# Kernel tuning notes

Measured on AMD Instinct MI355X. Metric: run time of the kernel, lower is better.

Reference implementation:

```python
import jax, jax.numpy as jnp
import numpy as np

N_NODES = 40000
N_EDGES = 640000
C = 128        # in_channels == hidden_channels
H = 8          # heads
D = C // H     # head dim = 16
L = 2          # num HGTConv layers
OUT = 64       # final fc out_channels


def _segment_softmax(logits, seg, num_segments):
    # logits: [E, H], seg: [E] destination ids
    m = jax.ops.segment_max(logits, seg, num_segments=num_segments)
    m = jnp.where(jnp.isfinite(m), m, 0.0)  # empty segments -> 0
    e = jnp.exp(logits - m[seg])
    s = jax.ops.segment_sum(e, seg, num_segments=num_segments)
    return e / (s[seg] + 1e-16)


def setup_inputs() -> dict:
    key = jax.random.key(0)
    ks = jax.random.split(key, 20)
    p = lambda k, shape, s=0.05: (jax.random.normal(k, shape, jnp.float32) * s)
    x = jax.random.normal(ks[0], (N_NODES, C), jnp.float32)
    edge_index = jax.random.randint(ks[1], (2, N_EDGES), 0, N_NODES, jnp.int64)
    return {
        "x": x,
        "edge_index": edge_index,
        # per-layer stacked params (all layers have C->C dims)
        "Wk": p(ks[2], (L, C, C)), "bk": jnp.zeros((L, C), jnp.float32),
        "Wq": p(ks[3], (L, C, C)), "bq": jnp.zeros((L, C), jnp.float32),
        "Wv": p(ks[4], (L, C, C)), "bv": jnp.zeros((L, C), jnp.float32),
        "a_rel": p(ks[5], (L, H, D, D), 0.1),  # relation key transform
        "m_rel": p(ks[6], (L, H, D, D), 0.1),  # relation message transform
        "p_rel": jnp.ones((L, H), jnp.float32),  # relation prior per head
        "skip": jnp.ones((L,), jnp.float32),      # skip gate logits
        "aW": p(ks[7], (L, C, C)), "ab": jnp.zeros((L, C), jnp.float32),
        "fcW": p(ks[8], (C, OUT)), "fcb": jnp.zeros((OUT,), jnp.float32),
    }


def reference(x, edge_index, Wk, bk, Wq, bq, Wv, bv, a_rel, m_rel, p_rel, skip,
              aW, ab, fcW, fcb):
    src, dst = edge_index[0], edge_index[1]
    n = x.shape[0]
    n_layers, heads, d = a_rel.shape[0], a_rel.shape[1], a_rel.shape[2]
    inv_sqrt_d = 1.0 / np.sqrt(d).astype(np.float32)

    h = x
    for l in range(n_layers):
        k = (h @ Wk[l] + bk[l]).reshape(n, heads, d)
        q = (h @ Wq[l] + bq[l]).reshape(n, heads, d)
        v = (h @ Wv[l] + bv[l]).reshape(n, heads, d)
        # relation-specific transforms applied at node level (single edge type)
        k2 = jnp.einsum('nhd,hde->nhe', k, a_rel[l])
        v2 = jnp.einsum('nhd,hde->nhe', v, m_rel[l])
        # per-edge attention logits [E, H]
        logits = jnp.sum(q[dst] * k2[src], axis=-1) * p_rel[l] * inv_sqrt_d
        alpha = _segment_softmax(logits, dst, n)                 # [E, H]
        msg = v2[src] * alpha[:, :, None]                        # [E, H, D]
        agg = jax.ops.segment_sum(msg, dst, num_segments=n)      # [N, H, D]
        agg = agg.reshape(n, heads * d)
        a = jax.nn.gelu(agg) @ aW[l] + ab[l]
        beta = jax.nn.sigmoid(skip[l])
        h = beta * a + (1.0 - beta) * h     # HGT skip (dims match)
        h = jax.nn.relu(h)                  # model-level relu
    return h @ fcW + fcb
```

## Files before the change

### kernel.cpp

```cpp
#include <hip/hip_runtime.h>
#include <hip/hip_bf16.h>
#include <math.h>

#define NN 40000
#define NE 640000

typedef __attribute__((ext_vector_type(8))) short short8;
typedef __attribute__((ext_vector_type(8))) unsigned short u16x8;
typedef __attribute__((ext_vector_type(4))) float f32x4;
typedef _Float16 h16x2 __attribute__((ext_vector_type(2)));

#define WBLOCKS 547
#define GBLOCKS 625
#define NCO 157
#define P1B 160
#define EPB 4000
#define NH (NCO*P1B)
#define NHB 99

#if __has_builtin(__builtin_amdgcn_fdot2)
#define HAS_FDOT2 1
#else
#define HAS_FDOT2 0
#endif

__device__ __forceinline__ float gelu_tanh(float x) {
    float x3 = x * x * x;
    float u = 0.7978845608028654f * (x + 0.044715f * x3);
    return 0.5f * x * (1.0f + tanhf(u));
}

__device__ __forceinline__ unsigned short f2bf(float v) {
    __hip_bfloat16 h = __float2bfloat16(v);
    return *reinterpret_cast<unsigned short*>(&h);
}

__device__ __forceinline__ unsigned short f2h(float v) {
    union { _Float16 h; unsigned short u; } c;
    c.h = (_Float16)v;
    return c.u;
}

__device__ __forceinline__ float bf2f(unsigned short u) {
    union { unsigned int i; float f; } c;
    c.i = ((unsigned int)u) << 16;
    return c.f;
}

__device__ __forceinline__ void unpack8(u16x8 u, float* f) {
    union { u16x8 v; unsigned int d[4]; } c; c.v = u;
    #pragma unroll
    for (int i = 0; i < 4; ++i) {
        union { unsigned int i_; float f_; } lo, hi;
        lo.i_ = c.d[i] << 16;
        hi.i_ = c.d[i] & 0xffff0000u;
        f[2 * i] = lo.f_;
        f[2 * i + 1] = hi.f_;
    }
}

union kv8 { u16x8 u; h16x2 p[4]; _Float16 h[8]; };
union frag8 { short8 s; unsigned short u[8]; u16x8 v; };

__global__ __launch_bounds__(256) void prep_kernel(
    const float* __restrict__ Wq, const float* __restrict__ bq,
    const float* __restrict__ Wk, const float* __restrict__ bk,
    const float* __restrict__ a_rel,
    const float* __restrict__ Wv, const float* __restrict__ bv,
    const float* __restrict__ m_rel,
    const float* __restrict__ p_rel,
    const float* __restrict__ aW, const float* __restrict__ fcW,
    unsigned short* __restrict__ BfT, float* __restrict__ biasf,
    unsigned short* __restrict__ aWT, unsigned short* __restrict__ fcWT,
    const int* __restrict__ eidx, int* __restrict__ Hmat)
{
    if (blockIdx.x >= WBLOCKS) {
        __shared__ int chist[NCO];
        int b = blockIdx.x - WBLOCKS;
        int t = threadIdx.x;
        if (t < NCO) chist[t] = 0;
        __syncthreads();
        int base = b * EPB;
        for (int e = base + t; e < base + EPB; e += 256)
            atomicAdd(&chist[eidx[NE + e] >> 8], 1);
        __syncthreads();
        if (t < NCO) Hmat[t * P1B + b] = chist[t];
        return;
    }
    int idx = blockIdx.x * 256 + threadIdx.x;
    if (idx < 2 * 129 * 384) {
        int l = idx / (129 * 384);
        int j = idx - l * (129 * 384);
        int r = j / 384;
        int col = j - r * 384;
        const float* Wq_l = Wq + l * 16384;
        const float* Wk_l = Wk + l * 16384;
        const float* Wv_l = Wv + l * 16384;
        const float* ar_l = a_rel + l * 2048;
        const float* mr_l = m_rel + l * 2048;
        float val;
        if (col < 128) {
            val = (r < 128) ? Wq_l[r * 128 + col] : bq[l * 128 + col];
        } else if (col < 256) {
            int cc = col - 128; int h = cc >> 4; int eo = cc & 15;
            float scale = p_rel[l * 8 + h] * 0.25f * 1.4426950408889634f;
            float s = 0.f;
            #pragma unroll
            for (int d = 0; d < 16; ++d) {
                float w = (r < 128) ? Wk_l[r * 128 + h * 16 + d] : bk[l * 128 + h * 16 + d];
                s += w * ar_l[h * 256 + d * 16 + eo];
            }
            val = s * scale;
        } else {
            int cc = col - 256; int h = cc >> 4; int eo = cc & 15;
            float s = 0.f;
            #pragma unroll
            for (int d = 0; d < 16; ++d) {
                float w = (r < 128) ? Wv_l[r * 128 + h * 16 + d] : bv[l * 128 + h * 16 + d];
                s += w * mr_l[h * 256 + d * 16 + eo];
            }
            val = s;
        }
        if (r < 128) BfT[(size_t)l * 49152 + (size_t)col * 128 + r] = f2bf(val);
        else         biasf[l * 384 + col] = val;
    } else if (idx < 2 * 129 * 384 + 2 * 16384) {
        int i = idx - 2 * 129 * 384;
        int l = i >> 14; int j = i & 16383;
        int r = j >> 7, c = j & 127;
        aWT[(size_t)l * 16384 + (size_t)c * 128 + r] = f2bf(aW[(size_t)l * 16384 + r * 128 + c]);
    } else {
        int i = idx - (2 * 129 * 384 + 2 * 16384);
        int c = i >> 7, r = i & 127;
        fcWT[(size_t)c * 128 + r] = f2bf(fcW[(size_t)r * 64 + c]);
    }
}

__global__ __launch_bounds__(256) void scan_blocks_kernel(
    const int* __restrict__ in, int* __restrict__ out, int* __restrict__ bsum)
{
    __shared__ int s[256];
    int t = threadIdx.x;
    int i = blockIdx.x * 256 + t;
    int v = (i < NH) ? in[i] : 0;
    s[t] = v;
    __syncthreads();
    #pragma unroll
    for (int off = 1; off < 256; off <<= 1) {
        int u = (t >= off) ? s[t - off] : 0;
        __syncthreads();
        s[t] += u;
        __syncthreads();
    }
    if (i < NH) out[i] = s[t] - v;
    if (t == 255) bsum[blockIdx.x] = s[255];
}

__global__ __launch_bounds__(256) void scan_top_kernel(
    const int* __restrict__ bsum, int* __restrict__ boffs)
{
    __shared__ int s[256];
    int t = threadIdx.x;
    int v = (t < NHB) ? bsum[t] : 0;
    s[t] = v;
    __syncthreads();
    #pragma unroll
    for (int off = 1; off < 256; off <<= 1) {
        int u = (t >= off) ? s[t - off] : 0;
        __syncthreads();
        s[t] += u;
        __syncthreads();
    }
    boffs[t] = s[t] - v;
}

__global__ __launch_bounds__(256) void scan_add_kernel(
    int* __restrict__ out, const int* __restrict__ boffs)
{
    int i = blockIdx.x * 256 + threadIdx.x;
    if (i < NH) out[i] += boffs[blockIdx.x];
}

__global__ __launch_bounds__(256) void pass2_kernel(
    const int* __restrict__ eidx, const int* __restrict__ O, int* __restrict__ ebuk)
{
    __shared__ int cur[NCO];
    int b = blockIdx.x, t = threadIdx.x;
    if (t < NCO) cur[t] = O[t * P1B + b];
    __syncthreads();
    int base = b * EPB;
    for (int e = base + t; e < base + EPB; e += 256) {
        int s = eidx[e];
        int d = eidx[NE + e];
        int pos = atomicAdd(&cur[d >> 8], 1);
        ebuk[pos] = ((d & 255) << 16) | s;
    }
}

__global__ __launch_bounds__(256) void qkv0_p3_kernel(
    const float* __restrict__ Af, const unsigned short* __restrict__ BT,
    const float* __restrict__ bias,
    unsigned short* __restrict__ qb, unsigned short* __restrict__ kvb,
    const int* __restrict__ O, const int* __restrict__ ebuk,
    int* __restrict__ deg, int* __restrict__ offs, int* __restrict__ srcSorted)
{
    if (blockIdx.x >= GBLOCKS) {
        __shared__ int hist[256], loffs[256], cur[256];
        int c = blockIdx.x - GBLOCKS;
        int t = threadIdx.x;
        int base = O[c * P1B];
        int end = (c < NCO - 1) ? O[(c + 1) * P1B] : NE;
        hist[t] = 0;
        __syncthreads();
        for (int i = base + t; i < end; i += 256)
            atomicAdd(&hist[ebuk[i] >> 16], 1);
        __syncthreads();
        int v = hist[t];
        loffs[t] = v;
        __syncthreads();
        #pragma unroll
        for (int off = 1; off < 256; off <<= 1) {
            int u = (t >= off) ? loffs[t - off] : 0;
            __syncthreads();
            loffs[t] += u;
            __syncthreads();
        }
        int excl = loffs[t] - v;
        int n = c * 256 + t;
        if (n < NN) { deg[n] = v; offs[n] = base + excl; }
        cur[t] = excl;
        __syncthreads();
        for (int i = base + t; i < end; i += 256) {
            int p = ebuk[i];
            int pos = atomicAdd(&cur[p >> 16], 1);
            srcSorted[base + pos] = p & 0xffff;
        }
        return;
    }
    __shared__ unsigned short Bs[64][136];
    int t = threadIdx.x;
    int row0 = blockIdx.x * 64;
    int w = t >> 6;
    int lr = t & 15;
    int quad = (t & 63) >> 4;
    int row = row0 + w * 16 + lr;

    frag8 af[4];
    {
        const float* ap = Af + (size_t)row * 128 + quad * 8;
        #pragma unroll
        for (int kc = 0; kc < 4; ++kc) {
            float4 a0 = *(const float4*)(ap + kc * 32);
            float4 a1 = *(const float4*)(ap + kc * 32 + 4);
            af[kc].u[0] = f2bf(a0.x); af[kc].u[1] = f2bf(a0.y);
            af[kc].u[2] = f2bf(a0.z); af[kc].u[3] = f2bf(a0.w);
            af[kc].u[4] = f2bf(a1.x); af[kc].u[5] = f2bf(a1.y);
            af[kc].u[6] = f2bf(a1.z); af[kc].u[7] = f2bf(a1.w);
        }
    }

    #pragma unroll
    for (int ct = 0; ct < 6; ++ct) {
        if (ct) __syncthreads();
        #pragma unroll
        for (int i = 0; i < 4; ++i) {
            int idx = t + i * 256;
            int r = idx >> 4;
            int c8 = (idx & 15) * 8;
            *(u16x8*)(&Bs[r][c8]) = *(const u16x8*)(BT + (size_t)(ct * 64 + r) * 128 + c8);
        }
        __syncthreads();
        f32x4 acc[4] = {{0.f,0.f,0.f,0.f},{0.f,0.f,0.f,0.f},
                        {0.f,0.f,0.f,0.f},{0.f,0.f,0.f,0.f}};
        #pragma unroll
        for (int kc = 0; kc < 4; ++kc) {
            #pragma unroll
            for (int n4 = 0; n4 < 4; ++n4) {
                short8 bfr = *(const short8*)(&Bs[n4 * 16 + lr][kc * 32 + quad * 8]);
                acc[n4] = __builtin_amdgcn_mfma_f32_16x16x32_bf16(bfr, af[kc].s, acc[n4], 0, 0, 0);
            }
        }
        unsigned short* dst = (ct < 2) ? (qb + (size_t)row * 128 + (ct & 1) * 64)
                                       : (kvb + (size_t)row * 256 + (ct - 2) * 64);
        #pragma unroll
        for (int n4 = 0; n4 < 4; ++n4) {
            int colb = n4 * 16 + quad * 4;
            float4 bv = *(const float4*)(bias + ct * 64 + colb);
            ushort4 o;
            if (ct >= 4) {
                o.x = f2bf(acc[n4][0] + bv.x);
                o.y = f2bf(acc[n4][1] + bv.y);
                o.z = f2bf(acc[n4][2] + bv.z);
                o.w = f2bf(acc[n4][3] + bv.w);
            } else {
                o.x = f2h(acc[n4][0] + bv.x);
                o.y = f2h(acc[n4][1] + bv.y);
                o.z = f2h(acc[n4][2] + bv.z);
                o.w = f2h(acc[n4][3] + bv.w);
            }
            *(ushort4*)(dst + colb) = o;
        }
    }
}

template <int HPFMT, int P2>
__global__ __launch_bounds__(256) void fused_kernel(
    const unsigned short* __restrict__ aggb,
    const unsigned short* __restrict__ aWT, const float* __restrict__ ab,
    const float* __restrict__ skip_p,
    const float* __restrict__ HprevF, const unsigned short* __restrict__ HprevB,
    unsigned short* __restrict__ hb_out,
    const unsigned short* __restrict__ W2T, const float* __restrict__ bias2,
    unsigned short* __restrict__ qb, unsigned short* __restrict__ kvb,
    float* __restrict__ outF)
{
    __shared__ unsigned short As[64][136];
    __shared__ unsigned short Bs[64][136];
    int t = threadIdx.x;
    int row0 = blockIdx.x * 64;
    int w = t >> 6;
    int lr = t & 15;
    int quad = (t & 63) >> 4;
    int row = row0 + w * 16 + lr;

    frag8 agf[4];
    {
        const unsigned short* ap = aggb + (size_t)row * 128 + quad * 8;
        #pragma unroll
        for (int kc = 0; kc < 4; ++kc) {
            u16x8 u = *(const u16x8*)(ap + kc * 32);
            #pragma unroll
            for (int j = 0; j < 8; ++j) agf[kc].u[j] = f2bf(gelu_tanh(bf2f(u[j])));
        }
    }

    float sv = skip_p[0];
    float beta = 1.f / (1.f + expf(-sv));
    float omb = 1.f - beta;

    f32x4 hacc[2][4];
    #pragma unroll
    for (int ct = 0; ct < 2; ++ct) {
        if (ct) __syncthreads();
        #pragma unroll
        for (int i = 0; i < 4; ++i) {
            int idx = t + i * 256;
            int r = idx >> 4;
            int c8 = (idx & 15) * 8;
            *(u16x8*)(&Bs[r][c8]) = *(const u16x8*)(aWT + (size_t)(ct * 64 + r) * 128 + c8);
        }
        __syncthreads();
        #pragma unroll
        for (int n4 = 0; n4 < 4; ++n4) hacc[ct][n4] = (f32x4){0.f,0.f,0.f,0.f};
        #pragma unroll
        for (int kc = 0; kc < 4; ++kc) {
            #pragma unroll
            for (int n4 = 0; n4 < 4; ++n4) {
                short8 bfr = *(const short8*)(&Bs[n4 * 16 + lr][kc * 32 + quad * 8]);
                hacc[ct][n4] = __builtin_amdgcn_mfma_f32_16x16x32_bf16(bfr, agf[kc].s, hacc[ct][n4], 0, 0, 0);
            }
        }
    }

    #pragma unroll
    for (int ct = 0; ct < 2; ++ct) {
        #pragma unroll
        for (int n4 = 0; n4 < 4; ++n4) {
            int colb = ct * 64 + n4 * 16 + quad * 4;
            float4 bv = *(const float4*)(ab + colb);
            float hp[4];
            if (HPFMT == 0) {
                float4 h4 = *(const float4*)(HprevF + (size_t)row * 128 + colb);
                hp[0] = h4.x; hp[1] = h4.y; hp[2] = h4.z; hp[3] = h4.w;
            } else {
                ushort4 h4 = *(const ushort4*)(HprevB + (size_t)row * 128 + colb);
                hp[0] = bf2f(h4.x); hp[1] = bf2f(h4.y); hp[2] = bf2f(h4.z); hp[3] = bf2f(h4.w);
            }
            ushort4 o;
            o.x = f2bf(fmaxf(beta * (hacc[ct][n4][0] + bv.x) + omb * hp[0], 0.f));
            o.y = f2bf(fmaxf(beta * (hacc[ct][n4][1] + bv.y) + omb * hp[1], 0.f));
            o.z = f2bf(fmaxf(beta * (hacc[ct][n4][2] + bv.z) + omb * hp[2], 0.f));
            o.w = f2bf(fmaxf(beta * (hacc[ct][n4][3] + bv.w) + omb * hp[3], 0.f));
            *(ushort4*)(&As[w * 16 + lr][colb]) = o;
            if (P2 == 0) *(ushort4*)(hb_out + (size_t)row * 128 + colb) = o;
        }
    }
    __syncthreads();

    if (P2 == 0) {
        #pragma unroll
        for (int ct = 0; ct < 6; ++ct) {
            if (ct) __syncthreads();
            #pragma unroll
            for (int i = 0; i < 4; ++i) {
                int idx = t + i * 256;
                int r = idx >> 4;
                int c8 = (idx & 15) * 8;
                *(u16x8*)(&Bs[r][c8]) = *(const u16x8*)(W2T + (size_t)(ct * 64 + r) * 128 + c8);
            }
            __syncthreads();
            f32x4 acc[4] = {{0.f,0.f,0.f,0.f},{0.f,0.f,0.f,0.f},
                            {0.f,0.f,0.f,0.f},{0.f,0.f,0.f,0.f}};
            #pragma unroll
            for (int kc = 0; kc < 4; ++kc) {
                short8 afr = *(const short8*)(&As[w * 16 + lr][kc * 32 + quad * 8]);
                #pragma unroll
                for (int n4 = 0; n4 < 4; ++n4) {
                    short8 bfr = *(const short8*)(&Bs[n4 * 16 + lr][kc * 32 + quad * 8]);
                    acc[n4] = __builtin_amdgcn_mfma_f32_16x16x32_bf16(bfr, afr, acc[n4], 0, 0, 0);
                }
            }
            unsigned short* dst = (ct < 2) ? (qb + (size_t)row * 128 + (ct & 1) * 64)
                                           : (kvb + (size_t)row * 256 + (ct - 2) * 64);
            #pragma unroll
            for (int n4 = 0; n4 < 4; ++n4) {
                int colb = n4 * 16 + quad * 4;
                float4 bv = *(const float4*)(bias2 + ct * 64 + colb);
                ushort4 o;
                if (ct >= 4) {
                    o.x = f2bf(acc[n4][0] + bv.x);
                    o.y = f2bf(acc[n4][1] + bv.y);
                    o.z = f2bf(acc[n4][2] + bv.z);
                    o.w = f2bf(acc[n4][3] + bv.w);
                } else {
                    o.x = f2h(acc[n4][0] + bv.x);
                    o.y = f2h(acc[n4][1] + bv.y);
                    o.z = f2h(acc[n4][2] + bv.z);
                    o.w = f2h(acc[n4][3] + bv.w);
                }
                *(ushort4*)(dst + colb) = o;
            }
        }
    } else {
        #pragma unroll
        for (int i = 0; i < 4; ++i) {
            int idx = t + i * 256;
            int r = idx >> 4;
            int c8 = (idx & 15) * 8;
            *(u16x8*)(&Bs[r][c8]) = *(const u16x8*)(W2T + (size_t)r * 128 + c8);
        }
        __syncthreads();
        f32x4 acc[4] = {{0.f,0.f,0.f,0.f},{0.f,0.f,0.f,0.f},
                        {0.f,0.f,0.f,0.f},{0.f,0.f,0.f,0.f}};
        #pragma unroll
        for (int kc = 0; kc < 4; ++kc) {
            short8 afr = *(const short8*)(&As[w * 16 + lr][kc * 32 + quad * 8]);
            #pragma unroll
            for (int n4 = 0; n4 < 4; ++n4) {
                short8 bfr = *(const short8*)(&Bs[n4 * 16 + lr][kc * 32 + quad * 8]);
                acc[n4] = __builtin_amdgcn_mfma_f32_16x16x32_bf16(bfr, afr, acc[n4], 0, 0, 0);
            }
        }
        #pragma unroll
        for (int n4 = 0; n4 < 4; ++n4) {
            int colb = n4 * 16 + quad * 4;
            float4 bv = *(const float4*)(bias2 + colb);
            float4 o;
            o.x = acc[n4][0] + bv.x;
            o.y = acc[n4][1] + bv.y;
            o.z = acc[n4][2] + bv.z;
            o.w = acc[n4][3] + bv.w;
            *(float4*)(outF + (size_t)row * 64 + colb) = o;
        }
    }
}

__global__ __launch_bounds__(256) void aggregate_kernel(
    const unsigned short* __restrict__ qb, const unsigned short* __restrict__ kvb,
    const int* __restrict__ deg, const int* __restrict__ offs,
    const int* __restrict__ srcSorted, unsigned short* __restrict__ aggb)
{
    int n = (blockIdx.x * 256 + threadIdx.x) >> 6;
    int lane = threadIdx.x & 63;
    int es = lane >> 3;
    int h = lane & 7;

#if HAS_FDOT2
    h16x2 q2[8];
    {
        const h16x2* qp = (const h16x2*)(qb + (size_t)n * 128 + h * 16);
        #pragma unroll
        for (int j = 0; j < 8; ++j) q2[j] = qp[j];
    }
#else
    float q[16];
    {
        kv8 a, b;
        a.u = *(const u16x8*)(qb + (size_t)n * 128 + h * 16);
        b.u = *(const u16x8*)(qb + (size_t)n * 128 + h * 16 + 8);
        #pragma unroll
        for (int j = 0; j < 8; ++j) { q[j] = (float)a.h[j]; q[8 + j] = (float)b.h[j]; }
    }
#endif
    float acc[16];
    #pragma unroll
    for (int j = 0; j < 16; ++j) acc[j] = 0.f;
    float den = 0.f;

    int start = offs[n];
    int d = deg[n];
    if (d > 0) {
        int ng = (d + 7) >> 3;
        int lastIdx = start + d - 1;

        kv8 ka0, ka1; u16x8 vA0, vA1;
        kv8 kB0, kB1; u16x8 vB0, vB1;
        {
            int i0 = start + es; if (i0 > lastIdx) i0 = lastIdx;
            const unsigned short* p = kvb + (size_t)srcSorted[i0] * 256 + h * 16;
            ka0.u = *(const u16x8*)p;        ka1.u = *(const u16x8*)(p + 8);
            vA0 = *(const u16x8*)(p + 128);  vA1 = *(const u16x8*)(p + 136);
        }
        kB0 = ka0; kB1 = ka1; vB0 = vA0; vB1 = vA1;
        if (ng > 1) {
            int i1 = start + 8 + es; if (i1 > lastIdx) i1 = lastIdx;
            const unsigned short* p = kvb + (size_t)srcSorted[i1] * 256 + h * 16;
            kB0.u = *(const u16x8*)p;        kB1.u = *(const u16x8*)(p + 8);
            vB0 = *(const u16x8*)(p + 128);  vB1 = *(const u16x8*)(p + 136);
        }

        for (int g = 0; g < ng; ++g) {
            kv8 kC0 = ka0, kC1 = ka1; u16x8 vC0 = vA0, vC1 = vA1;
            if (g + 2 < ng) {
                int ni = start + (g + 2) * 8 + es; if (ni > lastIdx) ni = lastIdx;
                const unsigned short* p = kvb + (size_t)srcSorted[ni] * 256 + h * 16;
                kC0.u = *(const u16x8*)p;        kC1.u = *(const u16x8*)(p + 8);
                vC0 = *(const u16x8*)(p + 128);  vC1 = *(const u16x8*)(p + 136);
            }
            float pdot = 0.f;
#if HAS_FDOT2
            #pragma unroll
            for (int j = 0; j < 4; ++j) pdot = __builtin_amdgcn_fdot2(ka0.p[j], q2[j], pdot, false);
            #pragma unroll
            for (int j = 0; j < 4; ++j) pdot = __builtin_amdgcn_fdot2(ka1.p[j], q2[4 + j], pdot, false);
#else
            #pragma unroll
            for (int j = 0; j < 8; ++j) pdot = fmaf((float)ka0.h[j], q[j], pdot);
            #pragma unroll
            for (int j = 0; j < 8; ++j) pdot = fmaf((float)ka1.h[j], q[8 + j], pdot);
#endif
            float ev = (g * 8 + es < d) ? exp2f(pdot) : 0.f;
            den += ev;
            float vf[16];
            unpack8(vA0, vf); unpack8(vA1, vf + 8);
            #pragma unroll
            for (int j = 0; j < 16; ++j) acc[j] = fmaf(vf[j], ev, acc[j]);
            ka0 = kB0; ka1 = kB1; vA0 = vB0; vA1 = vB1;
            kB0 = kC0; kB1 = kC1; vB0 = vC0; vB1 = vC1;
        }
    }
    #pragma unroll
    for (int m = 8; m < 64; m <<= 1) {
        den += __shfl_xor(den, m, 64);
        #pragma unroll
        for (int j = 0; j < 16; ++j) acc[j] += __shfl_xor(acc[j], m, 64);
    }
    if (es == 0) {
        float w = 1.f / (den + 1e-16f);
        u16x8 o0, o1;
        #pragma unroll
        for (int j = 0; j < 8; ++j) {
            o0[j] = f2bf(acc[j] * w);
            o1[j] = f2bf(acc[j + 8] * w);
        }
        *(u16x8*)(aggb + (size_t)n * 128 + h * 16) = o0;
        *(u16x8*)(aggb + (size_t)n * 128 + h * 16 + 8) = o1;
    }
}

extern "C" void kernel_launch(void* const* d_in, const int* in_sizes, int n_in,
                              void* d_out, int out_size, void* d_ws, size_t ws_size,
                              hipStream_t stream) {
    const float* x     = (const float*)d_in[0];
    const int*   eidx  = (const int*)d_in[1];
    const float* Wk    = (const float*)d_in[2];
    const float* bk    = (const float*)d_in[3];
    const float* Wq    = (const float*)d_in[4];
    const float* bq    = (const float*)d_in[5];
    const float* Wv    = (const float*)d_in[6];
    const float* bv    = (const float*)d_in[7];
    const float* a_rel = (const float*)d_in[8];
    const float* m_rel = (const float*)d_in[9];
    const float* p_rel = (const float*)d_in[10];
    const float* skip  = (const float*)d_in[11];
    const float* aW    = (const float*)d_in[12];
    const float* ab    = (const float*)d_in[13];
    const float* fcW   = (const float*)d_in[14];
    const float* fcb   = (const float*)d_in[15];
    float* out = (float*)d_out;

    float* biasf = (float*)d_ws;
    unsigned short* hb   = (unsigned short*)(biasf + 768);
    unsigned short* qb   = hb + (size_t)NN * 128;
    unsigned short* kvb  = qb + (size_t)NN * 128;
    unsigned short* aggb = kvb + (size_t)NN * 256;
    unsigned short* BfT  = aggb + (size_t)NN * 128;
    unsigned short* aWT  = BfT + 2 * 384 * 128;
    unsigned short* fcWT = aWT + 2 * 128 * 128;
    int* deg       = (int*)(fcWT + 64 * 128);
    int* offs      = deg + NN;
    int* Hmat      = offs + NN;
    int* bsum      = Hmat + NH;
    int* boffs     = bsum + 256;
    int* Oarr      = boffs + 256;
    int* ebuk      = Oarr + NH;
    int* srcSorted = ebuk + NE;

    prep_kernel<<<WBLOCKS + P1B, 256, 0, stream>>>(
        Wq, bq, Wk, bk, a_rel, Wv, bv, m_rel, p_rel, aW, fcW,
        BfT, biasf, aWT, fcWT, eidx, Hmat);
    scan_blocks_kernel<<<NHB, 256, 0, stream>>>(Hmat, Oarr, bsum);
    scan_top_kernel<<<1, 256, 0, stream>>>(bsum, boffs);
    scan_add_kernel<<<NHB, 256, 0, stream>>>(Oarr, boffs);
    pass2_kernel<<<P1B, 256, 0, stream>>>(eidx, Oarr, ebuk);

    qkv0_p3_kernel<<<GBLOCKS + NCO, 256, 0, stream>>>(
        x, BfT, biasf, qb, kvb, Oarr, ebuk, deg, offs, srcSorted);
    aggregate_kernel<<<NN / 4, 256, 0, stream>>>(qb, kvb, deg, offs, srcSorted, aggb);

    fused_kernel<0, 0><<<GBLOCKS, 256, 0, stream>>>(
        aggb, aWT, ab, skip, x, nullptr, hb,
        BfT + 49152, biasf + 384, qb, kvb, nullptr);
    aggregate_kernel<<<NN / 4, 256, 0, stream>>>(qb, kvb, deg, offs, srcSorted, aggb);

    fused_kernel<1, 2><<<GBLOCKS, 256, 0, stream>>>(
        aggb, aWT + 16384, ab + 128, skip + 1, nullptr, hb, nullptr,
        fcWT, fcb, nullptr, nullptr, out);
}
```

Measured before the change: 269.8 us.

## Read GEMM weight fragments directly from global memory and use exp2-based GELU

Removes the shared-memory staging of the transposed weight matrices (and their barriers) in the projection and fused kernels, so each wave loads its B fragments straight from global memory, relying on L1/L2 caching of the small weights. It also rewrites the tanh-GELU as x*sigmoid(2u) using a clamped exp2f instead of tanhf. This cuts LDS traffic, barriers and LDS footprint, which may raise occupancy, but adds redundant global loads across waves with latency exposed directly to the MFMA chain.

```diff
diff --git a/kernel.cpp b/kernel.cpp
--- a/kernel.cpp
+++ b/kernel.cpp
@@ -25,9 +25,11 @@
 #endif
 
 __device__ __forceinline__ float gelu_tanh(float x) {
-    float x3 = x * x * x;
-    float u = 0.7978845608028654f * (x + 0.044715f * x3);
-    return 0.5f * x * (1.0f + tanhf(u));
+    float u = 0.7978845608028654f * (x + 0.044715f * x * x * x);
+    float a = 2.885390081777927f * u;
+    a = fminf(fmaxf(a, -120.f), 120.f);
+    float E = exp2f(a);
+    return x * E / (E + 1.0f);
 }
 
 __device__ __forceinline__ unsigned short f2bf(float v) {
@@ -236,7 +238,6 @@
         }
         return;
     }
-    __shared__ unsigned short Bs[64][136];
     int t = threadIdx.x;
     int row0 = blockIdx.x * 64;
     int w = t >> 6;
@@ -260,22 +261,13 @@
 
     #pragma unroll
     for (int ct = 0; ct < 6; ++ct) {
-        if (ct) __syncthreads();
-        #pragma unroll
-        for (int i = 0; i < 4; ++i) {
-            int idx = t + i * 256;
-            int r = idx >> 4;
-            int c8 = (idx & 15) * 8;
-            *(u16x8*)(&Bs[r][c8]) = *(const u16x8*)(BT + (size_t)(ct * 64 + r) * 128 + c8);
-        }
-        __syncthreads();
         f32x4 acc[4] = {{0.f,0.f,0.f,0.f},{0.f,0.f,0.f,0.f},
                         {0.f,0.f,0.f,0.f},{0.f,0.f,0.f,0.f}};
         #pragma unroll
         for (int kc = 0; kc < 4; ++kc) {
             #pragma unroll
             for (int n4 = 0; n4 < 4; ++n4) {
-                short8 bfr = *(const short8*)(&Bs[n4 * 16 + lr][kc * 32 + quad * 8]);
+                short8 bfr = *(const short8*)(BT + (size_t)(ct * 64 + n4 * 16 + lr) * 128 + kc * 32 + quad * 8);
                 acc[n4] = __builtin_amdgcn_mfma_f32_16x16x32_bf16(bfr, af[kc].s, acc[n4], 0, 0, 0);
             }
         }
@@ -314,7 +306,6 @@
     float* __restrict__ outF)
 {
     __shared__ unsigned short As[64][136];
-    __shared__ unsigned short Bs[64][136];
     int t = threadIdx.x;
     int row0 = blockIdx.x * 64;
     int w = t >> 6;
@@ -340,22 +331,13 @@
     f32x4 hacc[2][4];
     #pragma unroll
     for (int ct = 0; ct < 2; ++ct) {
-        if (ct) __syncthreads();
-        #pragma unroll
-        for (int i = 0; i < 4; ++i) {
-            int idx = t + i * 256;
-            int r = idx >> 4;
-            int c8 = (idx & 15) * 8;
-            *(u16x8*)(&Bs[r][c8]) = *(const u16x8*)(aWT + (size_t)(ct * 64 + r) * 128 + c8);
-        }
-        __syncthreads();
         #pragma unroll
         for (int n4 = 0; n4 < 4; ++n4) hacc[ct][n4] = (f32x4){0.f,0.f,0.f,0.f};
         #pragma unroll
         for (int kc = 0; kc < 4; ++kc) {
             #pragma unroll
             for (int n4 = 0; n4 < 4; ++n4) {
-                short8 bfr = *(const short8*)(&Bs[n4 * 16 + lr][kc * 32 + quad * 8]);
+                short8 bfr = *(const short8*)(aWT + (size_t)(ct * 64 + n4 * 16 + lr) * 128 + kc * 32 + quad * 8);
                 hacc[ct][n4] = __builtin_amdgcn_mfma_f32_16x16x32_bf16(bfr, agf[kc].s, hacc[ct][n4], 0, 0, 0);
             }
         }
@@ -389,15 +371,6 @@
     if (P2 == 0) {
         #pragma unroll
         for (int ct = 0; ct < 6; ++ct) {
-            if (ct) __syncthreads();
-            #pragma unroll
-            for (int i = 0; i < 4; ++i) {
-                int idx = t + i * 256;
-                int r = idx >> 4;
-                int c8 = (idx & 15) * 8;
-                *(u16x8*)(&Bs[r][c8]) = *(const u16x8*)(W2T + (size_t)(ct * 64 + r) * 128 + c8);
-            }
-            __syncthreads();
             f32x4 acc[4] = {{0.f,0.f,0.f,0.f},{0.f,0.f,0.f,0.f},
                             {0.f,0.f,0.f,0.f},{0.f,0.f,0.f,0.f}};
             #pragma unroll
@@ -405,7 +378,7 @@
                 short8 afr = *(const short8*)(&As[w * 16 + lr][kc * 32 + quad * 8]);
                 #pragma unroll
                 for (int n4 = 0; n4 < 4; ++n4) {
-                    short8 bfr = *(const short8*)(&Bs[n4 * 16 + lr][kc * 32 + quad * 8]);
+                    short8 bfr = *(const short8*)(W2T + (size_t)(ct * 64 + n4 * 16 + lr) * 128 + kc * 32 + quad * 8);
                     acc[n4] = __builtin_amdgcn_mfma_f32_16x16x32_bf16(bfr, afr, acc[n4], 0, 0, 0);
                 }
             }
@@ -431,14 +404,6 @@
             }
         }
     } else {
-        #pragma unroll
-        for (int i = 0; i < 4; ++i) {
-            int idx = t + i * 256;
-            int r = idx >> 4;
-            int c8 = (idx & 15) * 8;
-            *(u16x8*)(&Bs[r][c8]) = *(const u16x8*)(W2T + (size_t)r * 128 + c8);
-        }
-        __syncthreads();
         f32x4 acc[4] = {{0.f,0.f,0.f,0.f},{0.f,0.f,0.f,0.f},
                         {0.f,0.f,0.f,0.f},{0.f,0.f,0.f,0.f}};
         #pragma unroll
@@ -446,7 +411,7 @@
             short8 afr = *(const short8*)(&As[w * 16 + lr][kc * 32 + quad * 8]);
             #pragma unroll
             for (int n4 = 0; n4 < 4; ++n4) {
-                short8 bfr = *(const short8*)(&Bs[n4 * 16 + lr][kc * 32 + quad * 8]);
+                short8 bfr = *(const short8*)(W2T + (size_t)(n4 * 16 + lr) * 128 + kc * 32 + quad * 8);
                 acc[n4] = __builtin_amdgcn_mfma_f32_16x16x32_bf16(bfr, afr, acc[n4], 0, 0, 0);
             }
         }
```

New measurement: 336.4 us. 1.25x slower.
